# Kernel tuning notes

Measured on AMD Instinct MI355X. Metric: run time of the kernel, lower is better.

The kernel has to match this reference:

```python
import jax, jax.numpy as jnp
import numpy as np

HIDDEN = 1024
B, S = 4, 2048

def setup_inputs() -> dict:
    key = jax.random.key(0)
    k1, k2 = jax.random.split(key)
    hidden_states = jax.random.normal(k1, (B, S, HIDDEN), dtype=jnp.float32)
    # torch nn.Linear weight layout: [out_features, in_features]
    W_proj = jax.random.normal(k2, (3 * HIDDEN, HIDDEN), dtype=jnp.float32) * (1.0 / np.sqrt(HIDDEN))
    b_proj = jnp.zeros((3 * HIDDEN,), dtype=jnp.float32)
    return {"hidden_states": hidden_states, "W_proj": W_proj, "b_proj": b_proj}

def reference(hidden_states, W_proj, b_proj):
    h = hidden_states.shape[-1]
    # fused QKV projection: y = x @ W^T + b
    qkv = jnp.einsum('bsh,oh->bso', hidden_states, W_proj) + b_proj
    q, k, v = jnp.split(qkv, 3, axis=-1)  # each [B,S,H]
    scale = 1.0 / jnp.sqrt(jnp.asarray(h, dtype=q.dtype))
    scores = jnp.einsum('bqh,bkh->bqk', q, k) * scale  # [B,S,S]
    attn = jax.nn.softmax(scores, axis=-1)
    out = jnp.einsum('bqk,bkh->bqh', attn, v)
    return out
```

## Files before the change

kernel.cpp:

```cpp
#include <hip/hip_runtime.h>
#include <stdint.h>

#define HIDDEN 1024
#define BATCH  4
#define SEQ    2048
#define TOKENS (BATCH * SEQ)
#define QKVD   (3 * HIDDEN)

typedef unsigned short u16;
typedef __attribute__((ext_vector_type(8))) short   short8;
typedef __attribute__((ext_vector_type(8))) unsigned short ushort8;
typedef __attribute__((ext_vector_type(4))) float   floatx4;

__device__ __forceinline__ u16 f32_bf16_rne(float f) {
    unsigned int u = __float_as_uint(f);
    u += 0x7FFFu + ((u >> 16) & 1u);
    return (u16)(u >> 16);
}

__device__ __forceinline__ void gl16(const u16* g, u16* l) {
    __builtin_amdgcn_global_load_lds(
        (const __attribute__((address_space(1))) void*)g,
        (__attribute__((address_space(3))) void*)l, 16, 0, 0);
}

#define SYNC3() do { __builtin_amdgcn_sched_barrier(0); \
    asm volatile("s_waitcnt vmcnt(3)\n\ts_barrier" ::: "memory"); } while (0)
#define PBAR() do { __builtin_amdgcn_sched_barrier(0); \
    asm volatile("s_barrier" ::: "memory"); } while (0)
#define LG0() asm volatile("s_waitcnt lgkmcnt(0)" ::: "memory")
#define VM4() do { __builtin_amdgcn_sched_barrier(0); \
    asm volatile("s_waitcnt vmcnt(4)" ::: "memory"); } while (0)

__global__ __launch_bounds__(256) void cvt2_bf16_kernel(
        const float* __restrict__ sa, const float* __restrict__ sb,
        u16* __restrict__ da, u16* __restrict__ db, int n4a, int n4tot) {
    int i = blockIdx.x * 256 + threadIdx.x;
    if (i >= n4tot) return;
    float4 v;
    if (i < n4a) v = ((const float4*)sa)[i];
    else         v = ((const float4*)sb)[i - n4a];
    ushort4 o;
    o.x = f32_bf16_rne(v.x); o.y = f32_bf16_rne(v.y);
    o.z = f32_bf16_rne(v.z); o.w = f32_bf16_rne(v.w);
    if (i < n4a) ((ushort4*)da)[i] = o;
    else         ((ushort4*)db)[i - n4a] = o;
}

__global__ __launch_bounds__(512, 2) void gemm_qkv(
        const u16* __restrict__ A, const u16* __restrict__ B,
        u16* __restrict__ C, u16* __restrict__ Vt,
        const float* __restrict__ bias) {
    __shared__ __align__(16) u16 lds[2][2][(128 + 256) * 32];

    const int t    = threadIdx.x;
    const int lane = t & 63;
    const int wid  = t >> 6;
    const int wr   = wid >> 2;
    const int wc   = wid & 3;
    const int bm   = blockIdx.y * 128;
    const int bn   = blockIdx.x * 256;

    const int rA  = t >> 2;
    const int sl  = (t & 3) ^ ((rA >> 1) & 3);
    const u16* gA  = A + (size_t)(bm + rA) * 1024 + sl * 8;
    const u16* gB0 = B + (size_t)(bn + rA) * 1024 + sl * 8;
    const u16* gB1 = gB0 + (size_t)128 * 1024;

    const int fr = lane & 15;
    const int kc = lane >> 4;
    const int fo = ((kc ^ ((fr >> 1) & 3)) << 4);
    const int aoffB = (wr * 64 + fr) * 64 + fo;
    const int boffB = (wc * 64 + fr) * 64 + fo;

    floatx4 acc[4][4];
#pragma unroll
    for (int i = 0; i < 4; i++)
#pragma unroll
        for (int j = 0; j < 4; j++) acc[i][j] = (floatx4){0.f, 0.f, 0.f, 0.f};

    short8 bfr0, bfr1, bfr2, bfr3, va0, va1;

#define LDB4(BASE) \
    bfr0 = *(const short8*)((BASE) + boffB);        \
    bfr1 = *(const short8*)((BASE) + boffB + 1024); \
    bfr2 = *(const short8*)((BASE) + boffB + 2048); \
    bfr3 = *(const short8*)((BASE) + boffB + 3072);

#define MFMA2(MI, A0, A1) \
    __builtin_amdgcn_s_setprio(1); \
    acc[MI][0]     = __builtin_amdgcn_mfma_f32_16x16x32_bf16(A0, bfr0, acc[MI][0], 0, 0, 0); \
    acc[MI][1]     = __builtin_amdgcn_mfma_f32_16x16x32_bf16(A0, bfr1, acc[MI][1], 0, 0, 0); \
    acc[MI][2]     = __builtin_amdgcn_mfma_f32_16x16x32_bf16(A0, bfr2, acc[MI][2], 0, 0, 0); \
    acc[MI][3]     = __builtin_amdgcn_mfma_f32_16x16x32_bf16(A0, bfr3, acc[MI][3], 0, 0, 0); \
    acc[(MI)+1][0] = __builtin_amdgcn_mfma_f32_16x16x32_bf16(A1, bfr0, acc[(MI)+1][0], 0, 0, 0); \
    acc[(MI)+1][1] = __builtin_amdgcn_mfma_f32_16x16x32_bf16(A1, bfr1, acc[(MI)+1][1], 0, 0, 0); \
    acc[(MI)+1][2] = __builtin_amdgcn_mfma_f32_16x16x32_bf16(A1, bfr2, acc[(MI)+1][2], 0, 0, 0); \
    acc[(MI)+1][3] = __builtin_amdgcn_mfma_f32_16x16x32_bf16(A1, bfr3, acc[(MI)+1][3], 0, 0, 0); \
    __builtin_amdgcn_s_setprio(0);

#define ITER(BUF, SBUF, SCOL) { \
    const char* As0_ = (const char*)&lds[BUF][0][0]; \
    const char* Bs0_ = As0_ + 8192; \
    const char* As1_ = (const char*)&lds[BUF][1][0]; \
    const char* Bs1_ = As1_ + 8192; \
    gl16(gA + (SCOL),       (u16*)((char*)&lds[SBUF][0][0]    + wid * 1024)); \
    LDB4(Bs0_); \
    va0 = *(const short8*)(As0_ + aoffB); \
    va1 = *(const short8*)(As0_ + aoffB + 1024); \
    MFMA2(0, va0, va1); \
    gl16(gB0 + (SCOL),      (u16*)((char*)&lds[SBUF][0][4096] + wid * 1024)); \
    gl16(gB1 + (SCOL),      (u16*)((char*)&lds[SBUF][0][8192] + wid * 1024)); \
    va0 = *(const short8*)(As0_ + aoffB + 2048); \
    va1 = *(const short8*)(As0_ + aoffB + 3072); \
    MFMA2(2, va0, va1); \
    SYNC3(); \
    gl16(gA + (SCOL) + 32,  (u16*)((char*)&lds[SBUF][1][0]    + wid * 1024)); \
    LDB4(Bs1_); \
    va0 = *(const short8*)(As1_ + aoffB); \
    va1 = *(const short8*)(As1_ + aoffB + 1024); \
    MFMA2(0, va0, va1); \
    gl16(gB0 + (SCOL) + 32, (u16*)((char*)&lds[SBUF][1][4096] + wid * 1024)); \
    gl16(gB1 + (SCOL) + 32, (u16*)((char*)&lds[SBUF][1][8192] + wid * 1024)); \
    va0 = *(const short8*)(As1_ + aoffB + 2048); \
    va1 = *(const short8*)(As1_ + aoffB + 3072); \
    MFMA2(2, va0, va1); \
    SYNC3(); }

    gl16(gA,       (u16*)((char*)&lds[0][0][0]    + wid * 1024));
    gl16(gB0,      (u16*)((char*)&lds[0][0][4096] + wid * 1024));
    gl16(gB1,      (u16*)((char*)&lds[0][0][8192] + wid * 1024));
    gl16(gA + 32,  (u16*)((char*)&lds[0][1][0]    + wid * 1024));
    gl16(gB0 + 32, (u16*)((char*)&lds[0][1][4096] + wid * 1024));
    gl16(gB1 + 32, (u16*)((char*)&lds[0][1][8192] + wid * 1024));
    SYNC3();

    const int nk = 1024 >> 6;
    for (int kt = 0; kt < nk; kt += 2) {
        const int c1 = (kt + 1) << 6;
        const int c2 = (kt + 2 < nk ? (kt + 2) : (nk - 1)) << 6;
        ITER(0, 1, c1)
        ITER(1, 0, c2)
    }
    asm volatile("s_waitcnt vmcnt(0)" ::: "memory");

#undef ITER
#undef MFMA2
#undef LDB4

    const int crow0 = bm + wr * 64 + kc * 4;
    const int ccol0 = bn + wc * 64 + fr;
    float bv[4];
#pragma unroll
    for (int ni = 0; ni < 4; ni++) bv[ni] = bias[ccol0 + ni * 16];

    if (blockIdx.x < 8) {
#pragma unroll
        for (int mi = 0; mi < 4; mi++)
#pragma unroll
            for (int ni = 0; ni < 4; ni++)
#pragma unroll
                for (int r = 0; r < 4; r++)
                    C[(size_t)(crow0 + mi * 16 + r) * QKVD + (ccol0 + ni * 16)] =
                        f32_bf16_rne(acc[mi][ni][r] + bv[ni]);
    } else {
        __syncthreads();
        u16 (*TB)[258] = (u16(*)[258]) & lds[0][0][0];
        const int lr0 = wr * 64 + kc * 4;
        const int lc0 = wc * 64 + fr;
#pragma unroll
        for (int mi = 0; mi < 4; mi++)
#pragma unroll
            for (int ni = 0; ni < 4; ni++)
#pragma unroll
                for (int r = 0; r < 4; r++)
                    TB[lr0 + mi * 16 + r][lc0 + ni * 16] =
                        f32_bf16_rne(acc[mi][ni][r] + bv[ni]);
        __syncthreads();
        const int b  = bm >> 11;
        const int sb = bm & 2047;
        const int h0 = bn - 2048;
        for (int it = 0; it < 2; ++it) {
            const int task = it * 512 + t;
            const int h    = task & 255;
            const int s0   = (task >> 8) * 32;
            ushort8 v[4];
#pragma unroll
            for (int j8 = 0; j8 < 4; ++j8)
#pragma unroll
                for (int j = 0; j < 8; ++j)
                    v[j8][j] = TB[s0 + j8 * 8 + j][h];
            u16* dst = Vt + (size_t)(b * 1024 + h0 + h) * 2048 + sb + s0;
#pragma unroll
            for (int j8 = 0; j8 < 4; ++j8)
                *(ushort8*)(dst + j8 * 8) = v[j8];
        }
    }
}

template <int EPI, int WM>
__global__ __launch_bounds__(512, 2) void gemm_bt(
        const u16* __restrict__ A, const u16* __restrict__ B,
        void* __restrict__ Cv, const float* __restrict__ bias,
        int K, int lda, int ldb, int ldc,
        size_t sA, size_t sB, size_t sC, float scale) {
    constexpr int BM    = 2 * WM;
    constexpr int MIH   = WM / 32;
    constexpr int ASLAB = BM * 64;
    constexpr int BSLAB = 256 * 64;
    constexpr int BUFB  = 2 * ASLAB + 2 * BSLAB;
    __shared__ __align__(16) char lds[2][BUFB];

    const int t    = threadIdx.x;
    const int lane = t & 63;
    const int wid  = t >> 6;
    const int wr   = wid >> 2;
    const int wc   = wid & 3;
    const int bm   = blockIdx.y * BM;
    const int bn   = blockIdx.x * 256;

    const u16* Ab = A + (size_t)blockIdx.z * sA;
    const u16* Bb = B + (size_t)blockIdx.z * sB;

    const int r0 = t >> 2;
    const int sl = (t & 3) ^ ((r0 >> 1) & 3);
    const u16* gA0 = Ab + (size_t)(bm + r0) * lda + sl * 8;
    const u16* gA1 = gA0 + (size_t)128 * lda;
    const u16* gB0 = Bb + (size_t)(bn + r0) * ldb + sl * 8;
    const u16* gB1 = gB0 + (size_t)128 * ldb;

    const int fr  = lane & 15;
    const int kc  = lane >> 4;
    const int frb = fr * 64 + ((kc ^ ((fr >> 1) & 3)) << 4);

    floatx4 acc[2 * MIH][4];
#pragma unroll
    for (int i = 0; i < 2 * MIH; i++)
#pragma unroll
        for (int j = 0; j < 4; j++) acc[i][j] = (floatx4){0.f, 0.f, 0.f, 0.f};

    short8 aF[MIH][2], bLo[2][2], bHi[2][2];

    auto rdA = [&](short8 (&dst)[MIH][2], const char* bp, int miBase) {
#pragma unroll
        for (int m = 0; m < MIH; m++)
#pragma unroll
            for (int ks = 0; ks < 2; ks++)
                dst[m][ks] = *(const short8*)(bp + ks * ASLAB +
                    (wr * WM + (miBase + m) * 16) * 64 + frb);
    };
    auto rdB = [&](short8 (&dst)[2][2], const char* bp, int niBase) {
#pragma unroll
        for (int n = 0; n < 2; n++)
#pragma unroll
            for (int ks = 0; ks < 2; ks++)
                dst[n][ks] = *(const short8*)(bp + 2 * ASLAB + ks * BSLAB +
                    (wc * 64 + (niBase + n) * 16) * 64 + frb);
    };
    auto mf = [&](short8 (&av)[MIH][2], short8 (&bv)[2][2], int miB, int niB) {
        __builtin_amdgcn_s_setprio(1);
#pragma unroll
        for (int m = 0; m < MIH; m++)
#pragma unroll
            for (int n = 0; n < 2; n++)
#pragma unroll
                for (int ks = 0; ks < 2; ks++)
                    acc[miB + m][niB + n] = __builtin_amdgcn_mfma_f32_16x16x32_bf16(
                        av[m][ks], bv[n][ks], acc[miB + m][niB + n], 0, 0, 0);
        __builtin_amdgcn_s_setprio(0);
    };

#define STA(buf, ks, sc) do { \
    char* d = &lds[buf][(ks) * ASLAB] + wid * 1024; \
    gl16(gA0 + (sc) + (ks) * 32, (u16*)d); \
    if constexpr (WM == 128) gl16(gA1 + (sc) + (ks) * 32, (u16*)(d + 8192)); \
  } while (0)
#define STB(buf, ks, sc) do { \
    char* d = &lds[buf][2 * ASLAB + (ks) * BSLAB] + wid * 1024; \
    gl16(gB0 + (sc) + (ks) * 32, (u16*)d); \
    gl16(gB1 + (sc) + (ks) * 32, (u16*)(d + 8192)); \
  } while (0)

#define GROUP(q, S1, S2, S3, S4) { \
    const char* bp = &lds[q][0]; \
    rdA(aF, bp, 0); rdB(bLo, bp, 0); S1; PBAR(); LG0(); \
    mf(aF, bLo, 0, 0);   PBAR(); \
    rdB(bHi, bp, 2);                S2; PBAR(); LG0(); \
    mf(aF, bHi, 0, 2);   PBAR(); \
    rdA(aF, bp, MIH);               S3; PBAR(); LG0(); \
    mf(aF, bHi, MIH, 2); PBAR(); \
    S4; VM4(); PBAR(); \
    mf(aF, bLo, MIH, 0); PBAR(); \
}

    STA(0, 0, 0); STA(0, 1, 0); STB(0, 0, 0); STB(0, 1, 0);
    STB(1, 0, 64); STB(1, 1, 64);
    VM4(); PBAR();

    const int nk = K >> 6;
    for (int T = 0; T < nk; T += 2) {
        const int c1 = (T + 1) << 6;
        const int c2 = (T + 2 < nk ? T + 2 : nk - 1) << 6;
        const int c3 = (T + 3 < nk ? T + 3 : nk - 1) << 6;
        GROUP(0, STA(1, 0, c1), STA(1, 1, c1), STB(0, 0, c2), STB(0, 1, c2))
        GROUP(1, STA(0, 0, c2), STA(0, 1, c2), STB(1, 0, c3), STB(1, 1, c3))
    }
    asm volatile("s_waitcnt vmcnt(0)" ::: "memory");

#undef GROUP
#undef STB
#undef STA

    const int crow0 = bm + wr * WM + kc * 4;
    const int ccol0 = bn + wc * 64 + fr;
    const size_t coff = (size_t)blockIdx.z * sC;

    float* C = (float*)Cv;
#pragma unroll
    for (int mi = 0; mi < 2 * MIH; mi++)
#pragma unroll
        for (int ni = 0; ni < 4; ni++)
#pragma unroll
            for (int r = 0; r < 4; r++) {
                float v = acc[mi][ni][r];
                if (EPI == 1) v *= scale;
                C[coff + (size_t)(crow0 + mi * 16 + r) * ldc + (ccol0 + ni * 16)] = v;
            }
}

__global__ __launch_bounds__(256) void softmax_kernel(
        const float* __restrict__ S, u16* __restrict__ P) {
    __shared__ float redm[4];
    __shared__ float reds[4];
    const size_t base = (size_t)blockIdx.x * SEQ;
    const int t = threadIdx.x, lane = t & 63, wid = t >> 6;
    const float4* src = (const float4*)(S + base);
    float4 a = src[t], b = src[t + 256];

    float m = fmaxf(fmaxf(fmaxf(a.x, a.y), fmaxf(a.z, a.w)),
                    fmaxf(fmaxf(b.x, b.y), fmaxf(b.z, b.w)));
#pragma unroll
    for (int off = 32; off; off >>= 1) m = fmaxf(m, __shfl_xor(m, off, 64));
    if (lane == 0) redm[wid] = m;
    __syncthreads();
    m = fmaxf(fmaxf(redm[0], redm[1]), fmaxf(redm[2], redm[3]));

    float e[8];
    e[0] = __expf(a.x - m); e[1] = __expf(a.y - m);
    e[2] = __expf(a.z - m); e[3] = __expf(a.w - m);
    e[4] = __expf(b.x - m); e[5] = __expf(b.y - m);
    e[6] = __expf(b.z - m); e[7] = __expf(b.w - m);
    float s = e[0] + e[1] + e[2] + e[3] + e[4] + e[5] + e[6] + e[7];
#pragma unroll
    for (int off = 32; off; off >>= 1) s += __shfl_xor(s, off, 64);
    if (lane == 0) reds[wid] = s;
    __syncthreads();
    s = reds[0] + reds[1] + reds[2] + reds[3];
    const float r = 1.f / s;

    ushort4* dst = (ushort4*)(P + base);
    ushort4 o0, o1;
    o0.x = f32_bf16_rne(e[0] * r); o0.y = f32_bf16_rne(e[1] * r);
    o0.z = f32_bf16_rne(e[2] * r); o0.w = f32_bf16_rne(e[3] * r);
    o1.x = f32_bf16_rne(e[4] * r); o1.y = f32_bf16_rne(e[5] * r);
    o1.z = f32_bf16_rne(e[6] * r); o1.w = f32_bf16_rne(e[7] * r);
    dst[t] = o0;
    dst[t + 256] = o1;
}

extern "C" void kernel_launch(void* const* d_in, const int* in_sizes, int n_in,
                              void* d_out, int out_size, void* d_ws, size_t ws_size,
                              hipStream_t stream) {
    const float* x    = (const float*)d_in[0];
    const float* W    = (const float*)d_in[1];
    const float* bias = (const float*)d_in[2];
    float* out = (float*)d_out;

    u16* Xb  = (u16*)d_ws;
    u16* Wb  = Xb + (size_t)TOKENS * HIDDEN;
    u16* qkv = Wb + (size_t)QKVD * HIDDEN;
    float* scores = (float*)(qkv + (size_t)TOKENS * QKVD);
    u16* P  = (u16*)(scores + (size_t)BATCH * SEQ * SEQ);
    u16* Vt = P + (size_t)BATCH * SEQ * SEQ;

    {
        const int n4a = TOKENS * HIDDEN / 4;
        const int n4b = QKVD * HIDDEN / 4;
        const int n4t = n4a + n4b;
        cvt2_bf16_kernel<<<(n4t + 255) / 256, 256, 0, stream>>>(x, W, Xb, Wb, n4a, n4t);
    }

    gemm_qkv<<<dim3(QKVD / 256, TOKENS / 128, 1), 512, 0, stream>>>(
        Xb, Wb, qkv, Vt, bias);

    gemm_bt<1, 128><<<dim3(SEQ / 256, SEQ / 256, BATCH), 512, 0, stream>>>(
        qkv, qkv + HIDDEN, scores, nullptr, HIDDEN, QKVD, QKVD, SEQ,
        (size_t)SEQ * QKVD, (size_t)SEQ * QKVD, (size_t)SEQ * SEQ, 0.03125f);

    softmax_kernel<<<BATCH * SEQ, 256, 0, stream>>>(scores, P);

    gemm_bt<2, 64><<<dim3(HIDDEN / 256, SEQ / 128, BATCH), 512, 0, stream>>>(
        P, Vt, out, nullptr, SEQ, SEQ, SEQ, HIDDEN,
        (size_t)SEQ * SEQ, (size_t)HIDDEN * SEQ, (size_t)SEQ * HIDDEN, 1.f);
}
```

Baseline: 259.3 us.

## Move V transpose from QKV GEMM epilogue into softmax kernel blocks

The QKV GEMM no longer transposes the V slice through LDS in its epilogue. It now writes all of Q, K and V uniformly to the qkv buffer. The softmax launch gets 2048 extra blocks that read V from qkv, transpose 64x64 tiles through padded shared memory, and write Vt. The aim is to remove the divergent, LDS-heavy epilogue path from the GEMM and hide the transpose inside the memory-bound softmax launch. The cost is an extra read of V from global memory and scalar 16-bit accesses in the transpose blocks.

```diff
diff --git a/kernel.cpp b/kernel.cpp
--- a/kernel.cpp
+++ b/kernel.cpp
@@ -9,7 +9,6 @@
 
 typedef unsigned short u16;
 typedef __attribute__((ext_vector_type(8))) short   short8;
-typedef __attribute__((ext_vector_type(8))) unsigned short ushort8;
 typedef __attribute__((ext_vector_type(4))) float   floatx4;
 
 __device__ __forceinline__ u16 f32_bf16_rne(float f) {
@@ -49,8 +48,7 @@
 
 __global__ __launch_bounds__(512, 2) void gemm_qkv(
         const u16* __restrict__ A, const u16* __restrict__ B,
-        u16* __restrict__ C, u16* __restrict__ Vt,
-        const float* __restrict__ bias) {
+        u16* __restrict__ C, const float* __restrict__ bias) {
     __shared__ __align__(16) u16 lds[2][2][(128 + 256) * 32];
 
     const int t    = threadIdx.x;
@@ -153,49 +151,14 @@
     float bv[4];
 #pragma unroll
     for (int ni = 0; ni < 4; ni++) bv[ni] = bias[ccol0 + ni * 16];
-
-    if (blockIdx.x < 8) {
-#pragma unroll
-        for (int mi = 0; mi < 4; mi++)
-#pragma unroll
-            for (int ni = 0; ni < 4; ni++)
-#pragma unroll
-                for (int r = 0; r < 4; r++)
-                    C[(size_t)(crow0 + mi * 16 + r) * QKVD + (ccol0 + ni * 16)] =
-                        f32_bf16_rne(acc[mi][ni][r] + bv[ni]);
-    } else {
-        __syncthreads();
-        u16 (*TB)[258] = (u16(*)[258]) & lds[0][0][0];
-        const int lr0 = wr * 64 + kc * 4;
-        const int lc0 = wc * 64 + fr;
-#pragma unroll
-        for (int mi = 0; mi < 4; mi++)
-#pragma unroll
-            for (int ni = 0; ni < 4; ni++)
-#pragma unroll
-                for (int r = 0; r < 4; r++)
-                    TB[lr0 + mi * 16 + r][lc0 + ni * 16] =
-                        f32_bf16_rne(acc[mi][ni][r] + bv[ni]);
-        __syncthreads();
-        const int b  = bm >> 11;
-        const int sb = bm & 2047;
-        const int h0 = bn - 2048;
-        for (int it = 0; it < 2; ++it) {
-            const int task = it * 512 + t;
-            const int h    = task & 255;
-            const int s0   = (task >> 8) * 32;
-            ushort8 v[4];
-#pragma unroll
-            for (int j8 = 0; j8 < 4; ++j8)
-#pragma unroll
-                for (int j = 0; j < 8; ++j)
-                    v[j8][j] = TB[s0 + j8 * 8 + j][h];
-            u16* dst = Vt + (size_t)(b * 1024 + h0 + h) * 2048 + sb + s0;
-#pragma unroll
-            for (int j8 = 0; j8 < 4; ++j8)
-                *(ushort8*)(dst + j8 * 8) = v[j8];
-        }
-    }
+#pragma unroll
+    for (int mi = 0; mi < 4; mi++)
+#pragma unroll
+        for (int ni = 0; ni < 4; ni++)
+#pragma unroll
+            for (int r = 0; r < 4; r++)
+                C[(size_t)(crow0 + mi * 16 + r) * QKVD + (ccol0 + ni * 16)] =
+                    f32_bf16_rne(acc[mi][ni][r] + bv[ni]);
 }
 
 template <int EPI, int WM>
@@ -328,44 +291,67 @@
             }
 }
 
-__global__ __launch_bounds__(256) void softmax_kernel(
-        const float* __restrict__ S, u16* __restrict__ P) {
+__global__ __launch_bounds__(256) void softmax_tr_kernel(
+        const float* __restrict__ S, u16* __restrict__ P,
+        const u16* __restrict__ qkv, u16* __restrict__ Vt) {
     __shared__ float redm[4];
     __shared__ float reds[4];
-    const size_t base = (size_t)blockIdx.x * SEQ;
-    const int t = threadIdx.x, lane = t & 63, wid = t >> 6;
-    const float4* src = (const float4*)(S + base);
-    float4 a = src[t], b = src[t + 256];
-
-    float m = fmaxf(fmaxf(fmaxf(a.x, a.y), fmaxf(a.z, a.w)),
-                    fmaxf(fmaxf(b.x, b.y), fmaxf(b.z, b.w)));
-#pragma unroll
-    for (int off = 32; off; off >>= 1) m = fmaxf(m, __shfl_xor(m, off, 64));
-    if (lane == 0) redm[wid] = m;
-    __syncthreads();
-    m = fmaxf(fmaxf(redm[0], redm[1]), fmaxf(redm[2], redm[3]));
-
-    float e[8];
-    e[0] = __expf(a.x - m); e[1] = __expf(a.y - m);
-    e[2] = __expf(a.z - m); e[3] = __expf(a.w - m);
-    e[4] = __expf(b.x - m); e[5] = __expf(b.y - m);
-    e[6] = __expf(b.z - m); e[7] = __expf(b.w - m);
-    float s = e[0] + e[1] + e[2] + e[3] + e[4] + e[5] + e[6] + e[7];
-#pragma unroll
-    for (int off = 32; off; off >>= 1) s += __shfl_xor(s, off, 64);
-    if (lane == 0) reds[wid] = s;
-    __syncthreads();
-    s = reds[0] + reds[1] + reds[2] + reds[3];
-    const float r = 1.f / s;
-
-    ushort4* dst = (ushort4*)(P + base);
-    ushort4 o0, o1;
-    o0.x = f32_bf16_rne(e[0] * r); o0.y = f32_bf16_rne(e[1] * r);
-    o0.z = f32_bf16_rne(e[2] * r); o0.w = f32_bf16_rne(e[3] * r);
-    o1.x = f32_bf16_rne(e[4] * r); o1.y = f32_bf16_rne(e[5] * r);
-    o1.z = f32_bf16_rne(e[6] * r); o1.w = f32_bf16_rne(e[7] * r);
-    dst[t] = o0;
-    dst[t + 256] = o1;
+    __shared__ u16 tile[64][66];
+    const int t = threadIdx.x;
+
+    if ((int)blockIdx.x < TOKENS) {
+        const size_t base = (size_t)blockIdx.x * SEQ;
+        const int lane = t & 63, wid = t >> 6;
+        const float4* src = (const float4*)(S + base);
+        float4 a = src[t], b = src[t + 256];
+
+        float m = fmaxf(fmaxf(fmaxf(a.x, a.y), fmaxf(a.z, a.w)),
+                        fmaxf(fmaxf(b.x, b.y), fmaxf(b.z, b.w)));
+#pragma unroll
+        for (int off = 32; off; off >>= 1) m = fmaxf(m, __shfl_xor(m, off, 64));
+        if (lane == 0) redm[wid] = m;
+        __syncthreads();
+        m = fmaxf(fmaxf(redm[0], redm[1]), fmaxf(redm[2], redm[3]));
+
+        float e[8];
+        e[0] = __expf(a.x - m); e[1] = __expf(a.y - m);
+        e[2] = __expf(a.z - m); e[3] = __expf(a.w - m);
+        e[4] = __expf(b.x - m); e[5] = __expf(b.y - m);
+        e[6] = __expf(b.z - m); e[7] = __expf(b.w - m);
+        float s = e[0] + e[1] + e[2] + e[3] + e[4] + e[5] + e[6] + e[7];
+#pragma unroll
+        for (int off = 32; off; off >>= 1) s += __shfl_xor(s, off, 64);
+        if (lane == 0) reds[wid] = s;
+        __syncthreads();
+        s = reds[0] + reds[1] + reds[2] + reds[3];
+        const float r = 1.f / s;
+
+        ushort4* dst = (ushort4*)(P + base);
+        ushort4 o0, o1;
+        o0.x = f32_bf16_rne(e[0] * r); o0.y = f32_bf16_rne(e[1] * r);
+        o0.z = f32_bf16_rne(e[2] * r); o0.w = f32_bf16_rne(e[3] * r);
+        o1.x = f32_bf16_rne(e[4] * r); o1.y = f32_bf16_rne(e[5] * r);
+        o1.z = f32_bf16_rne(e[6] * r); o1.w = f32_bf16_rne(e[7] * r);
+        dst[t] = o0;
+        dst[t + 256] = o1;
+    } else {
+        const int bx = blockIdx.x - TOKENS;
+        const int b  = bx >> 9;
+        const int s0 = (bx & 31) * 64;
+        const int h0 = ((bx >> 5) & 15) * 64;
+        const int c = t & 63, r4 = t >> 6;
+#pragma unroll
+        for (int i = 0; i < 16; i++) {
+            int sl = i * 4 + r4;
+            tile[sl][c] = qkv[(size_t)(b * SEQ + s0 + sl) * QKVD + 2 * HIDDEN + h0 + c];
+        }
+        __syncthreads();
+#pragma unroll
+        for (int i = 0; i < 16; i++) {
+            int hl = i * 4 + r4;
+            Vt[(size_t)(b * HIDDEN + h0 + hl) * SEQ + s0 + c] = tile[c][hl];
+        }
+    }
 }
 
 extern "C" void kernel_launch(void* const* d_in, const int* in_sizes, int n_in,
@@ -391,13 +377,13 @@
     }
 
     gemm_qkv<<<dim3(QKVD / 256, TOKENS / 128, 1), 512, 0, stream>>>(
-        Xb, Wb, qkv, Vt, bias);
+        Xb, Wb, qkv, bias);
 
     gemm_bt<1, 128><<<dim3(SEQ / 256, SEQ / 256, BATCH), 512, 0, stream>>>(
         qkv, qkv + HIDDEN, scores, nullptr, HIDDEN, QKVD, QKVD, SEQ,
         (size_t)SEQ * QKVD, (size_t)SEQ * QKVD, (size_t)SEQ * SEQ, 0.03125f);
 
-    softmax_kernel<<<BATCH * SEQ, 256, 0, stream>>>(scores, P);
+    softmax_tr_kernel<<<TOKENS + 2048, 256, 0, stream>>>(scores, P, qkv, Vt);
 
     gemm_bt<2, 64><<<dim3(HIDDEN / 256, SEQ / 128, BATCH), 512, 0, stream>>>(
         P, Vt, out, nullptr, SEQ, SEQ, SEQ, HIDDEN,
```

Measured after the change: 253.0 us. 2.4% less time.
